# Optimization experiments

Measured on AMD Instinct MI355X. Metric: run time of the kernel, lower is better.

Reference implementation:

```python
import jax, jax.numpy as jnp
import numpy as np

TEMPERATURE = 0.07


def _l2_normalize(x, axis=-1, eps=1e-12):
    # matches torch F.normalize: x / max(||x||, eps)
    n = jnp.sqrt(jnp.sum(x * x, axis=axis, keepdims=True))
    return x / jnp.maximum(n, eps)


def setup_inputs() -> dict:
    key = jax.random.key(0)
    k1, k2, k3 = jax.random.split(key, 3)
    B, C, H, W = 1024, 256, 24, 24
    img_features = jax.random.normal(k1, (B, C, H, W), dtype=jnp.float32)
    text_embeds = jax.random.normal(k2, (B, C), dtype=jnp.float32)
    labels = jax.random.randint(k3, (B,), 0, 16, dtype=jnp.int64)
    return {"img_features": img_features, "text_embeds": text_embeds, "labels": labels}


def reference(img_features, text_embeds, labels):
    # adaptive_avg_pool2d to 1x1 == global mean over H,W -> [B, C]
    img_pooled = img_features.mean(axis=(2, 3))
    img_pooled = _l2_normalize(img_pooled, axis=1)
    text_n = _l2_normalize(text_embeds, axis=1)
    logits = (img_pooled @ text_n.T) / TEMPERATURE  # [B, B]
    # vectorized label equality replaces the O(N^2) python loop
    targets = (labels[:, None] == labels[None, :]).astype(logits.dtype)
    # BCE with logits, mean reduction: logaddexp(0, x) - x*z
    loss = jnp.mean(jnp.logaddexp(0.0, logits) - logits * targets)
    return loss
```

## Files before the change

kernel.cpp:

```cpp
#include <hip/hip_runtime.h>
#include <math.h>

static constexpr int B_N  = 1024;
static constexpr int C_N  = 256;
static constexpr int HW_N = 576;
static constexpr float TEMP_INV = 1.0f / 0.07f;

typedef __attribute__((ext_vector_type(8))) short bf16x8;
typedef __attribute__((ext_vector_type(4))) float f32x4;

static __device__ __forceinline__ unsigned short f2bf(float f) {
    unsigned u = __float_as_uint(f);
    return (unsigned short)((u + 0x7FFFu + ((u >> 16) & 1u)) >> 16);
}

__global__ __launch_bounds__(1024) void fused_prep_kernel(const float* __restrict__ img,
                                                          const float* __restrict__ text,
                                                          unsigned short* __restrict__ Ab,
                                                          unsigned short* __restrict__ Bb,
                                                          float* __restrict__ loss_acc,
                                                          unsigned int* __restrict__ ticket) {
    __shared__ float means[C_N];
    const int t    = threadIdx.x;
    const int w    = t >> 6;
    const int lane = t & 63;

    if (blockIdx.x == 0 && t == 0) { *loss_acc = 0.0f; *ticket = 0u; }

    if (blockIdx.x < (unsigned)B_N) {
        const int b = blockIdx.x;
        #pragma unroll
        for (int ch = 0; ch < 16; ++ch) {
            const int c = (w << 4) + ch;
            const float4* src = (const float4*)(img + ((size_t)b * C_N + c) * HW_N);
            float s = 0.0f;
            #pragma unroll
            for (int it = 0; it < 3; ++it) {
                const int idx = lane + it * 64;
                if (idx < 144) {
                    const float4 v = src[idx];
                    s += (v.x + v.y) + (v.z + v.w);
                }
            }
            #pragma unroll
            for (int off = 32; off > 0; off >>= 1) s += __shfl_xor(s, off, 64);
            if (lane == 0) means[c] = s * (1.0f / (float)HW_N);
        }
        __syncthreads();
        if (w == 0) {
            const float4 v = ((const float4*)means)[lane];
            float ss = v.x * v.x + v.y * v.y + v.z * v.z + v.w * v.w;
            #pragma unroll
            for (int off = 32; off > 0; off >>= 1) ss += __shfl_xor(ss, off, 64);
            const float inv = 1.0f / fmaxf(sqrtf(ss), 1e-12f);
            ushort4 o;
            o.x = f2bf(v.x * inv); o.y = f2bf(v.y * inv);
            o.z = f2bf(v.z * inv); o.w = f2bf(v.w * inv);
            ((ushort4*)(Ab + (size_t)b * C_N))[lane] = o;
        }
    } else {
        const int rb = (blockIdx.x - B_N) * 64;
        #pragma unroll
        for (int rr = 0; rr < 4; ++rr) {
            const int r = rb + (w << 2) + rr;
            const float4 v = ((const float4*)(text + (size_t)r * C_N))[lane];
            float ss = v.x * v.x + v.y * v.y + v.z * v.z + v.w * v.w;
            #pragma unroll
            for (int off = 32; off > 0; off >>= 1) ss += __shfl_xor(ss, off, 64);
            const float inv = 1.0f / fmaxf(sqrtf(ss), 1e-12f);
            ushort4 o;
            o.x = f2bf(v.x * inv); o.y = f2bf(v.y * inv);
            o.z = f2bf(v.z * inv); o.w = f2bf(v.w * inv);
            ((ushort4*)(Bb + (size_t)r * C_N))[lane] = o;
        }
    }
}

__global__ __launch_bounds__(256) void gemm_loss_kernel(const unsigned short* __restrict__ Ab,
                                                        const unsigned short* __restrict__ Bb,
                                                        const int* __restrict__ labels,
                                                        float* __restrict__ loss_acc,
                                                        unsigned int* __restrict__ ticket,
                                                        float* __restrict__ out) {
    __shared__ unsigned short Abuf[64 * 256];
    __shared__ unsigned short Bbuf[64 * 256];

    const int t = threadIdx.x;
    const int rowBase = (blockIdx.x & 15) << 6;
    const int colBase = (blockIdx.x >> 4) << 6;

    #pragma unroll
    for (int i = 0; i < 8; ++i) {
        const int c   = t + (i << 8);
        const int row = c >> 5;
        const int kc  = c & 31;
        const unsigned off = (unsigned)((row << 9) + (kc << 4)) ^ (unsigned)((row & 7) << 4);
        uint4 va = ((const uint4*)(Ab + (size_t)(rowBase + row) * C_N))[kc];
        *(uint4*)((char*)Abuf + off) = va;
        uint4 vb = ((const uint4*)(Bb + (size_t)(colBase + row) * C_N))[kc];
        *(uint4*)((char*)Bbuf + off) = vb;
    }
    __syncthreads();

    const int w    = t >> 6;
    const int lane = t & 63;
    const int m16  = lane & 15;
    const int kg   = lane >> 4;

    f32x4 acc[4] = {{0.f, 0.f, 0.f, 0.f}, {0.f, 0.f, 0.f, 0.f},
                    {0.f, 0.f, 0.f, 0.f}, {0.f, 0.f, 0.f, 0.f}};

    #pragma unroll
    for (int s = 0; s < 8; ++s) {
        const int kc   = (s << 2) + kg;
        const int arow = (w << 4) + m16;
        const bf16x8 a = *(const bf16x8*)((char*)Abuf +
                            (((unsigned)((arow << 9) + (kc << 4))) ^ (unsigned)((arow & 7) << 4)));
        #pragma unroll
        for (int ct = 0; ct < 4; ++ct) {
            const int brow = (ct << 4) + m16;
            const bf16x8 b = *(const bf16x8*)((char*)Bbuf +
                                (((unsigned)((brow << 9) + (kc << 4))) ^ (unsigned)((brow & 7) << 4)));
            acc[ct] = __builtin_amdgcn_mfma_f32_16x16x32_bf16(a, b, acc[ct], 0, 0, 0);
        }
    }

    float lsum = 0.0f;
    const int gi0 = rowBase + (w << 4) + (kg << 2);
    int labi[4];
    #pragma unroll
    for (int r = 0; r < 4; ++r) labi[r] = labels[gi0 + r];
    #pragma unroll
    for (int ct = 0; ct < 4; ++ct) {
        const int gj = colBase + (ct << 4) + m16;
        const int labj = labels[gj];
        #pragma unroll
        for (int r = 0; r < 4; ++r) {
            const float x = acc[ct][r] * TEMP_INV;
            const float z = (labi[r] == labj) ? 1.0f : 0.0f;
            const float sp = fmaxf(x, 0.0f) + __logf(1.0f + __expf(-fabsf(x)));
            lsum += sp - x * z;
        }
    }

    #pragma unroll
    for (int off = 32; off > 0; off >>= 1) lsum += __shfl_xor(lsum, off, 64);
    __syncthreads();
    float* red = (float*)Abuf;
    if ((t & 63) == 0) red[w] = lsum;
    __syncthreads();
    if (t == 0) {
        const float bsum = red[0] + red[1] + red[2] + red[3];
        atomicAdd(loss_acc, bsum);
        __threadfence();
        const unsigned old = atomicAdd(ticket, 1u);
        if (old == 255u) {
            const float total = atomicAdd(loss_acc, 0.0f);
            out[0] = total * (1.0f / ((float)B_N * (float)B_N));
        }
    }
}

extern "C" void kernel_launch(void* const* d_in, const int* in_sizes, int n_in,
                              void* d_out, int out_size, void* d_ws, size_t ws_size,
                              hipStream_t stream) {
    const float* img    = (const float*)d_in[0];
    const float* text   = (const float*)d_in[1];
    const int*   labels = (const int*)d_in[2];
    float* out = (float*)d_out;

    char* ws = (char*)d_ws;
    unsigned short* Ab       = (unsigned short*)ws;
    unsigned short* Bb       = (unsigned short*)(ws + (512 << 10));
    float*          loss_acc = (float*)(ws + (1 << 20));
    unsigned int*   ticket   = (unsigned int*)(ws + (1 << 20) + 4);

    fused_prep_kernel<<<B_N + 16, 1024, 0, stream>>>(img, text, Ab, Bb, loss_acc, ticket);
    gemm_loss_kernel<<<256, 256, 0, stream>>>(Ab, Bb, labels, loss_acc, ticket, out);
}
```

Measured before the change: 119.5 us.

## Split pooling into many small blocks with nontemporal loads and separate normalize kernel

The pooling stage no longer uses one 1024-thread block per image. It now launches 16384 small blocks, each wave reducing 4 channels from 9 nontemporal float4 loads issued up front. Pooled means go to a float workspace, and a new small kernel normalizes them and converts to bf16. This aims to raise memory-level parallelism and occupancy on the dominant ~600MB read, at the cost of an extra kernel launch and a pooled round trip through global memory.

```diff
diff --git a/kernel.cpp b/kernel.cpp
--- a/kernel.cpp
+++ b/kernel.cpp
@@ -8,62 +8,30 @@
 
 typedef __attribute__((ext_vector_type(8))) short bf16x8;
 typedef __attribute__((ext_vector_type(4))) float f32x4;
+typedef __attribute__((ext_vector_type(4))) float f4v;
 
 static __device__ __forceinline__ unsigned short f2bf(float f) {
     unsigned u = __float_as_uint(f);
     return (unsigned short)((u + 0x7FFFu + ((u >> 16) & 1u)) >> 16);
 }
 
-__global__ __launch_bounds__(1024) void fused_prep_kernel(const float* __restrict__ img,
-                                                          const float* __restrict__ text,
-                                                          unsigned short* __restrict__ Ab,
-                                                          unsigned short* __restrict__ Bb,
-                                                          float* __restrict__ loss_acc,
-                                                          unsigned int* __restrict__ ticket) {
-    __shared__ float means[C_N];
+__global__ __launch_bounds__(256) void pool_kernel(const float* __restrict__ img,
+                                                   const float* __restrict__ text,
+                                                   float* __restrict__ pooled,
+                                                   unsigned short* __restrict__ Bb,
+                                                   float* __restrict__ loss_acc,
+                                                   unsigned int* __restrict__ ticket) {
     const int t    = threadIdx.x;
     const int w    = t >> 6;
     const int lane = t & 63;
 
-    if (blockIdx.x == 0 && t == 0) { *loss_acc = 0.0f; *ticket = 0u; }
-
-    if (blockIdx.x < (unsigned)B_N) {
-        const int b = blockIdx.x;
+    if (blockIdx.x < 32) {
+        if (blockIdx.x == 0 && t == 0) { *loss_acc = 0.0f; *ticket = 0u; }
+        const int r0 = blockIdx.x * 32 + w * 8;
         #pragma unroll
-        for (int ch = 0; ch < 16; ++ch) {
-            const int c = (w << 4) + ch;
-            const float4* src = (const float4*)(img + ((size_t)b * C_N + c) * HW_N);
-            float s = 0.0f;
-            #pragma unroll
-            for (int it = 0; it < 3; ++it) {
-                const int idx = lane + it * 64;
-                if (idx < 144) {
-                    const float4 v = src[idx];
-                    s += (v.x + v.y) + (v.z + v.w);
-                }
-            }
-            #pragma unroll
-            for (int off = 32; off > 0; off >>= 1) s += __shfl_xor(s, off, 64);
-            if (lane == 0) means[c] = s * (1.0f / (float)HW_N);
-        }
-        __syncthreads();
-        if (w == 0) {
-            const float4 v = ((const float4*)means)[lane];
-            float ss = v.x * v.x + v.y * v.y + v.z * v.z + v.w * v.w;
-            #pragma unroll
-            for (int off = 32; off > 0; off >>= 1) ss += __shfl_xor(ss, off, 64);
-            const float inv = 1.0f / fmaxf(sqrtf(ss), 1e-12f);
-            ushort4 o;
-            o.x = f2bf(v.x * inv); o.y = f2bf(v.y * inv);
-            o.z = f2bf(v.z * inv); o.w = f2bf(v.w * inv);
-            ((ushort4*)(Ab + (size_t)b * C_N))[lane] = o;
-        }
-    } else {
-        const int rb = (blockIdx.x - B_N) * 64;
-        #pragma unroll
-        for (int rr = 0; rr < 4; ++rr) {
-            const int r = rb + (w << 2) + rr;
-            const float4 v = ((const float4*)(text + (size_t)r * C_N))[lane];
+        for (int rr = 0; rr < 8; ++rr) {
+            const int r = r0 + rr;
+            const f4v v = ((const f4v*)(text + (size_t)r * C_N))[lane];
             float ss = v.x * v.x + v.y * v.y + v.z * v.z + v.w * v.w;
             #pragma unroll
             for (int off = 32; off > 0; off >>= 1) ss += __shfl_xor(ss, off, 64);
@@ -73,7 +41,57 @@
             o.z = f2bf(v.z * inv); o.w = f2bf(v.w * inv);
             ((ushort4*)(Bb + (size_t)r * C_N))[lane] = o;
         }
-    }
+        return;
+    }
+
+    const int g = blockIdx.x - 32;
+    const size_t ch4 = (size_t)g * 16 + (size_t)w * 4;
+    const f4v* src = (const f4v*)img + ch4 * 144;
+
+    f4v vv[9];
+    #pragma unroll
+    for (int j = 0; j < 9; ++j)
+        vv[j] = __builtin_nontemporal_load(&src[j * 64 + lane]);
+
+    float a0 = 0.f, a1 = 0.f, a2 = 0.f, a3 = 0.f;
+    #pragma unroll
+    for (int j = 0; j < 9; ++j) {
+        const int idx = j * 64 + lane;
+        const float s = (vv[j].x + vv[j].y) + (vv[j].z + vv[j].w);
+        a0 += (idx < 144)               ? s : 0.0f;
+        a1 += (idx >= 144 && idx < 288) ? s : 0.0f;
+        a2 += (idx >= 288 && idx < 432) ? s : 0.0f;
+        a3 += (idx >= 432)              ? s : 0.0f;
+    }
+
+    #pragma unroll
+    for (int off = 32; off > 0; off >>= 1) {
+        a0 += __shfl_xor(a0, off, 64);
+        a1 += __shfl_xor(a1, off, 64);
+        a2 += __shfl_xor(a2, off, 64);
+        a3 += __shfl_xor(a3, off, 64);
+    }
+    if (lane == 0) {
+        const float sc = 1.0f / (float)HW_N;
+        f4v o; o.x = a0 * sc; o.y = a1 * sc; o.z = a2 * sc; o.w = a3 * sc;
+        ((f4v*)pooled)[ch4 >> 2] = o;
+    }
+}
+
+__global__ __launch_bounds__(256) void prep_kernel(const float* __restrict__ pooled,
+                                                   unsigned short* __restrict__ Ab) {
+    const int w    = threadIdx.x >> 6;
+    const int lane = threadIdx.x & 63;
+    const int r = blockIdx.x * 4 + w;
+    const float4 v = ((const float4*)(pooled + (size_t)r * C_N))[lane];
+    float ss = v.x * v.x + v.y * v.y + v.z * v.z + v.w * v.w;
+    #pragma unroll
+    for (int off = 32; off > 0; off >>= 1) ss += __shfl_xor(ss, off, 64);
+    const float inv = 1.0f / fmaxf(sqrtf(ss), 1e-12f);
+    ushort4 o;
+    o.x = f2bf(v.x * inv); o.y = f2bf(v.y * inv);
+    o.z = f2bf(v.z * inv); o.w = f2bf(v.w * inv);
+    ((ushort4*)(Ab + (size_t)r * C_N))[lane] = o;
 }
 
 __global__ __launch_bounds__(256) void gemm_loss_kernel(const unsigned short* __restrict__ Ab,
@@ -172,9 +190,11 @@
     char* ws = (char*)d_ws;
     unsigned short* Ab       = (unsigned short*)ws;
     unsigned short* Bb       = (unsigned short*)(ws + (512 << 10));
-    float*          loss_acc = (float*)(ws + (1 << 20));
-    unsigned int*   ticket   = (unsigned int*)(ws + (1 << 20) + 4);
-
-    fused_prep_kernel<<<B_N + 16, 1024, 0, stream>>>(img, text, Ab, Bb, loss_acc, ticket);
+    float*          pooled   = (float*)(ws + (1 << 20));
+    float*          loss_acc = (float*)(ws + (2 << 20));
+    unsigned int*   ticket   = (unsigned int*)(ws + (2 << 20) + 4);
+
+    pool_kernel<<<32 + 16384, 256, 0, stream>>>(img, text, pooled, Bb, loss_acc, ticket);
+    prep_kernel<<<256, 256, 0, stream>>>(pooled, Ab);
     gemm_loss_kernel<<<256, 256, 0, stream>>>(Ab, Bb, labels, loss_acc, ticket, out);
 }
```

After: 108.7 us. -9.0%, faster.
